# Kernel tuning notes

Measured on AMD Instinct MI355X. Metric: run time of the kernel, lower is better.

Reference implementation:

```python
import jax, jax.numpy as jnp
import numpy as np

EPS = 1e-5

def bn(x, gamma, beta, axes):
    # training-mode batchnorm over `axes`, channel axis = 1 (matches nn.BatchNorm1d/2d)
    mean = jnp.mean(x, axis=axes, keepdims=True)
    var = jnp.var(x, axis=axes, keepdims=True)
    shp = [1] * x.ndim
    shp[1] = -1
    return gamma.reshape(shp) * (x - mean) * jax.lax.rsqrt(var + EPS) + beta.reshape(shp)

def setup_inputs():
    key = jax.random.key(0)
    B, N, K, Cin, Cout, m = 4, 4096, 32, 64, 64, 8
    ks = jax.random.split(key, 10)
    def w(k, shape, fan_in):
        return jax.random.normal(k, shape, jnp.float32) * np.float32(np.sqrt(2.0 / fan_in))
    return {
        "x": jax.random.normal(ks[0], (B, Cin, N), jnp.float32),
        "xyz_score": jax.random.normal(ks[1], (B, 66, N, K), jnp.float32),
        "conv1_w": w(ks[2], (Cin, Cin), Cin),
        "bn1_g": jnp.ones((Cin,), jnp.float32), "bn1_b": jnp.zeros((Cin,), jnp.float32),
        "matrice2": w(ks[3], (Cin, m * Cout), Cin),  # weight bank: i x (m*o)
        "sn_w0": w(ks[4], (64, 66), 66), "sn_g0": jnp.ones((64,), jnp.float32), "sn_b0": jnp.zeros((64,), jnp.float32),
        "sn_w1": w(ks[5], (32, 64), 64), "sn_g1": jnp.ones((32,), jnp.float32), "sn_b1": jnp.zeros((32,), jnp.float32),
        "sn_w2": w(ks[6], (16, 32), 32), "sn_g2": jnp.ones((16,), jnp.float32), "sn_b2": jnp.zeros((16,), jnp.float32),
        "sn_w3": w(ks[7], (m, 16), 16), "sn_bias3": jnp.zeros((m,), jnp.float32),
        "bn2_g": jnp.ones((Cout,), jnp.float32), "bn2_b": jnp.zeros((Cout,), jnp.float32),
        "idx": jax.random.randint(ks[8], (B, N, K), 0, N, dtype=jnp.int32),
    }

def reference(x, xyz_score, conv1_w, bn1_g, bn1_b, matrice2,
              sn_w0, sn_g0, sn_b0, sn_w1, sn_g1, sn_b1, sn_w2, sn_g2, sn_b2,
              sn_w3, sn_bias3, bn2_g, bn2_b, idx):
    B, Cin, N = x.shape
    m = sn_w3.shape[0]
    # conv1 (1x1, no bias) + BN1 + ReLU  -> [B, Cin, N]
    h = jnp.einsum('oc,bcn->bon', conv1_w, x)
    h = jax.nn.relu(bn(h, bn1_g, bn1_b, (0, 2)))
    # feat_trans_pointnet: [B,N,Cin] @ [Cin, m*Cout] -> [B,N,m,Cout]
    y = jnp.einsum('bcn,ck->bnk', h, matrice2).reshape(B, N, m, -1)
    # ScoreNet: stack of 1x1 conv2d + BN + ReLU, final conv with bias, softmax over m
    s = xyz_score  # [B, 66, N, K]
    s = jax.nn.relu(bn(jnp.einsum('oc,bcnk->bonk', sn_w0, s), sn_g0, sn_b0, (0, 2, 3)))
    s = jax.nn.relu(bn(jnp.einsum('oc,bcnk->bonk', sn_w1, s), sn_g1, sn_b1, (0, 2, 3)))
    s = jax.nn.relu(bn(jnp.einsum('oc,bcnk->bonk', sn_w2, s), sn_g2, sn_b2, (0, 2, 3)))
    s = jnp.einsum('oc,bcnk->bonk', sn_w3, s) + sn_bias3[None, :, None, None]
    score = jax.nn.softmax(s, axis=1)            # [B, m, N, K], bias=0
    score = jnp.transpose(score, (0, 2, 3, 1))   # [B, N, K, m]
    # assemble_pointnet: gather neighbor transformed feats and score-weight them
    neigh = y[jnp.arange(B)[:, None, None], idx]             # [B, N, K, m, Cout]
    out = jnp.einsum('bnkm,bnkmo->bon', score, neigh)        # [B, Cout, N]
    return jax.nn.relu(bn(out, bn2_g, bn2_b, (0, 2)))
```

## Files before the change

### kernel.cpp

```cpp
#include <hip/hip_runtime.h>
#include <cstdint>

typedef unsigned short u16;
typedef unsigned int   u32;
typedef __attribute__((ext_vector_type(8))) short short8;
typedef __attribute__((ext_vector_type(4))) float f32x4;

constexpr int CB = 4;
constexpr int CN = 4096;
constexpr int CK = 32;
constexpr int NPTS = CB * CN * CK;
constexpr int NBK  = 131072;
constexpr float EPSV = 1e-5f;

struct __align__(16) Q4 { u32 a, b, c, d; };

static __device__ __forceinline__ u16 f2b(float f) {
  union { float f; u32 u; } v; v.f = f;
  u32 u = v.u;
  return (u16)((u + 0x7FFFu + ((u >> 16) & 1u)) >> 16);
}
static __device__ __forceinline__ float b2f(u16 h) {
  union { u32 u; float f; } v; v.u = ((u32)h) << 16;
  return v.f;
}
static __device__ __forceinline__ u32 pk2(float lo, float hi) {
  return (u32)f2b(lo) | ((u32)f2b(hi) << 16);
}
static __device__ __forceinline__ short8 mk8(u32 a, u32 b, u32 c, u32 d) {
  union { u32 w[4]; short8 v; } u; u.w[0]=a; u.w[1]=b; u.w[2]=c; u.w[3]=d; return u.v;
}

__global__ __launch_bounds__(256) void k_conv1(const float* __restrict__ x,
                                               const float* __restrict__ w,
                                               float* __restrict__ h,
                                               float* S, float* Q) {
  __shared__ float wl[16 * 64];
  __shared__ float ls[32];
  int tid = threadIdx.x;
  int og = blockIdx.x >> 6;
  int cb = blockIdx.x & 63;
  for (int i = tid; i < 1024; i += 256) wl[i] = w[og * 1024 + i];
  if (tid < 32) ls[tid] = 0.f;
  __syncthreads();
  int col = cb * 256 + tid;
  int b = col >> 12, n = col & 4095;
  float xr[64];
  const float* xp = x + (size_t)(b * 64) * CN + n;
  #pragma unroll
  for (int c = 0; c < 64; ++c) xr[c] = xp[(size_t)c * CN];
  int lane = tid & 63;
  for (int oo = 0; oo < 16; ++oo) {
    int o = og * 16 + oo;
    float acc = 0.f;
    const float* wr = &wl[oo * 64];
    #pragma unroll
    for (int c = 0; c < 64; ++c) acc = fmaf(wr[c], xr[c], acc);
    h[(size_t)(b * 64 + o) * CN + n] = acc;
    float v = acc, v2 = acc * acc;
    for (int d = 1; d < 64; d <<= 1) { v += __shfl_xor(v, d); v2 += __shfl_xor(v2, d); }
    if (lane == 0) { atomicAdd(&ls[oo], v); atomicAdd(&ls[16 + oo], v2); }
  }
  __syncthreads();
  if (tid < 16) atomicAdd(&S[og * 16 + tid], ls[tid]);
  else if (tid < 32) atomicAdd(&Q[og * 16 + tid - 16], ls[tid]);
}

__global__ __launch_bounds__(64) void k_affine(const float* S, const float* Q,
                                               const float* g, const float* bt,
                                               float* A, float* Bo, int C, float inv_cnt) {
  int t = threadIdx.x;
  if (t < C) {
    float mean = S[t] * inv_cnt;
    float var = fmaxf(Q[t] * inv_cnt - mean * mean, 0.f);
    float a = g[t] * rsqrtf(var + EPSV);
    A[t] = a;
    Bo[t] = bt[t] - mean * a;
  }
}

__global__ __launch_bounds__(256) void k_prepM2(const float* __restrict__ M2,
                                                u16* __restrict__ m2frag) {
  int i = blockIdx.x * 256 + threadIdx.x;
  int e = i & 7, lane = (i >> 3) & 63, t = i >> 9;
  int mt = t >> 1, kc = t & 1;
  int row = 16 * mt + (lane & 15);
  int k = 32 * kc + 8 * (lane >> 4) + e;
  m2frag[i] = f2b(M2[k * 512 + row]);
}

__global__ __launch_bounds__(256) void k_y(const float* __restrict__ h,
                                           const u16* __restrict__ m2frag,
                                           const float* __restrict__ Ah,
                                           const float* __restrict__ Bh,
                                           u16* __restrict__ y16) {
  __shared__ u16 yl[4][16 * 520];
  __shared__ float abl[128];
  int tid = threadIdx.x;
  if (tid < 64) abl[tid] = Ah[tid];
  else if (tid < 128) abl[tid] = Bh[tid - 64];
  int wv = tid >> 6, lane = tid & 63, g = lane >> 4, pl = lane & 15;
  __syncthreads();
  int wid = blockIdx.x * 4 + wv;
  int n0 = wid * 16;
  int b = n0 >> 12, nloc = n0 & 4095;
  const float* sb = h + (size_t)(b * 64) * CN + nloc + pl;
  u32 w[8];
  #pragma unroll
  for (int kc = 0; kc < 2; ++kc) {
    #pragma unroll
    for (int e2 = 0; e2 < 4; ++e2) {
      int c0 = 32 * kc + 8 * g + 2 * e2;
      float v0 = fmaxf(fmaf(abl[c0],     sb[(size_t)c0 * CN],       abl[64 + c0]),     0.f);
      float v1 = fmaxf(fmaf(abl[c0 + 1], sb[(size_t)(c0 + 1) * CN], abl[64 + c0 + 1]), 0.f);
      w[kc * 4 + e2] = pk2(v0, v1);
    }
  }
  short8 Bf0 = mk8(w[0], w[1], w[2], w[3]);
  short8 Bf1 = mk8(w[4], w[5], w[6], w[7]);
  const short8* m2f = (const short8*)m2frag;
  u16* ylw = &yl[wv][0];
  #pragma unroll
  for (int mt = 0; mt < 32; ++mt) {
    short8 A0 = m2f[(mt * 2 + 0) * 64 + lane];
    short8 A1 = m2f[(mt * 2 + 1) * 64 + lane];
    f32x4 z = {0.f, 0.f, 0.f, 0.f};
    z = __builtin_amdgcn_mfma_f32_16x16x32_bf16(A0, Bf0, z, 0, 0, 0);
    z = __builtin_amdgcn_mfma_f32_16x16x32_bf16(A1, Bf1, z, 0, 0, 0);
    u32* wp = (u32*)&ylw[pl * 520 + 16 * mt + 4 * g];
    wp[0] = pk2(z[0], z[1]);
    wp[1] = pk2(z[2], z[3]);
  }
  u16* yg = y16 + (size_t)n0 * 512;
  for (int j = 0; j < 16; ++j) {
    short8 v = *(const short8*)&ylw[j * 520 + lane * 8];
    *(short8*)(yg + (size_t)j * 512 + lane * 8) = v;
  }
}

static __device__ __forceinline__ void ld_frags(const float* __restrict__ xyz,
                                                int c, int g, int pl, short8 fr[5]) {
  int pbase = c * 32;
  int b = pbase >> 17, r = pbase & (NBK - 1);
  const float* base = xyz + (size_t)b * 66 * NBK + r + g * 8;
  #pragma unroll
  for (int ci = 0; ci < 4; ++ci) {
    const float* p = base + (size_t)(16 * ci + pl) * NBK;
    float4 v0 = *(const float4*)p;
    float4 v1 = *(const float4*)(p + 4);
    fr[ci] = mk8(pk2(v0.x, v0.y), pk2(v0.z, v0.w), pk2(v1.x, v1.y), pk2(v1.z, v1.w));
  }
  if (pl < 2) {
    const float* p = base + (size_t)(64 + pl) * NBK;
    float4 v0 = *(const float4*)p;
    float4 v1 = *(const float4*)(p + 4);
    fr[4] = mk8(pk2(v0.x, v0.y), pk2(v0.z, v0.w), pk2(v1.x, v1.y), pk2(v1.z, v1.w));
  } else if (pl == 2) {
    fr[4] = mk8(0x3F803F80u, 0x3F803F80u, 0x3F803F80u, 0x3F803F80u);
  } else {
    fr[4] = mk8(0u, 0u, 0u, 0u);
  }
}

__global__ __launch_bounds__(256) void k_moment(const float* __restrict__ xyz,
                                                float* __restrict__ Mpart) {
  constexpr int TI[15] = {0,0,0,0,0,1,1,1,1,2,2,2,3,3,4};
  constexpr int TJ[15] = {0,1,2,3,4,1,2,3,4,2,3,4,3,4,4};
  int tid = threadIdx.x;
  int wv = tid >> 6;
  int wid = blockIdx.x * 4 + wv;
  int lane = tid & 63, g = lane >> 4, pl = lane & 15;
  f32x4 acc[15];
  #pragma unroll
  for (int t = 0; t < 15; ++t) acc[t] = (f32x4){0.f, 0.f, 0.f, 0.f};
  for (int cc = wid; cc < NPTS / 32; cc += 4096) {
    short8 fr0[5], fr1[5];
    ld_frags(xyz, cc,        g, pl, fr0);
    ld_frags(xyz, cc + 2048, g, pl, fr1);
    #pragma unroll
    for (int t = 0; t < 15; ++t)
      acc[t] = __builtin_amdgcn_mfma_f32_16x16x32_bf16(fr0[TI[t]], fr0[TJ[t]], acc[t], 0, 0, 0);
    #pragma unroll
    for (int t = 0; t < 15; ++t)
      acc[t] = __builtin_amdgcn_mfma_f32_16x16x32_bf16(fr1[TI[t]], fr1[TJ[t]], acc[t], 0, 0, 0);
  }
  float* mp = Mpart + (size_t)wid * 3840;
  #pragma unroll
  for (int t = 0; t < 15; ++t)
    *(f32x4*)(mp + t * 256 + lane * 4) = acc[t];
}

__global__ __launch_bounds__(256) void k_mreduce(const float* __restrict__ Mpart,
                                                 float* __restrict__ M) {
  int e = blockIdx.x * 256 + threadIdx.x;
  int kg = blockIdx.y;
  float s = 0.f;
  for (int k = kg * 256; k < kg * 256 + 256; ++k) s += Mpart[(size_t)k * 3840 + e];
  atomicAdd(&M[e], s);
}

__global__ __launch_bounds__(256) void k_affine1m(const float* __restrict__ M,
                                                  const float* __restrict__ w0,
                                                  const float* __restrict__ g0,
                                                  const float* __restrict__ b0,
                                                  float* __restrict__ A1,
                                                  float* __restrict__ B1) {
  __shared__ float lsM[67 * 68];
  __shared__ float w0l[64 * 69];
  __shared__ float red[4 * 64];
  int tid = threadIdx.x;
  const float inv = 1.f / (float)NPTS;
  for (int i = tid; i < 67 * 67; i += 256) {
    int r = i / 67, c = i % 67;
    int rr = r, cc = c;
    if ((r >> 4) > (c >> 4)) { rr = c; cc = r; }
    int ti = rr >> 4, tj = cc >> 4;
    int t = ti * (9 - ti) / 2 + tj;
    int rho = rr & 15, kap = cc & 15;
    lsM[r * 68 + c] = M[t * 256 + ((rho >> 2) * 16 + kap) * 4 + (rho & 3)] * inv;
  }
  for (int i = tid; i < 64 * 66; i += 256) {
    int o = i / 66, c = i % 66;
    w0l[o * 69 + c] = w0[i];
  }
  __syncthreads();
  int o = tid & 63, sl = tid >> 6;
  float acc2 = 0.f;
  for (int c1 = sl * 17; c1 < sl * 17 + 17; ++c1) {
    if (c1 >= 66) break;
    float inner = 0.f;
    const float* mr = &lsM[c1 * 68];
    const float* wr = &w0l[o * 69];
    for (int c2 = 0; c2 < 66; ++c2) inner = fmaf(mr[c2], wr[c2], inner);
    acc2 = fmaf(wr[c1], inner, acc2);
  }
  red[sl * 64 + o] = acc2;
  __syncthreads();
  if (sl == 0) {
    float Ez2 = red[o] + red[64 + o] + red[128 + o] + red[192 + o];
    float mean = 0.f;
    const float* wr = &w0l[o * 69];
    for (int c = 0; c < 66; ++c) mean = fmaf(wr[c], lsM[c * 68 + 66], mean);
    float var = fmaxf(Ez2 - mean * mean, 0.f);
    float a = g0[o] * rsqrtf(var + EPSV);
    A1[o] = a;
    B1[o] = b0[o] - mean * a;
  }
}

__global__ __launch_bounds__(256) void k_prep(const float* __restrict__ w0,
                                              const float* __restrict__ w1,
                                              const float* __restrict__ A1,
                                              const float* __restrict__ B1,
                                              u16* __restrict__ w0frag,
                                              u16* __restrict__ w1frag) {
  int tid = threadIdx.x;
  for (int i = tid; i < 6144; i += 256) {
    int e = i & 7, lane = (i >> 3) & 63, t = i >> 9;
    int mt = t / 3, kc = t % 3;
    int row = 16 * mt + (lane & 15);
    int k = 32 * kc + 8 * (lane >> 4) + e;
    float v;
    if (k < 66)      v = A1[row] * w0[row * 66 + k];
    else if (k == 66) v = B1[row];
    else              v = 0.f;
    w0frag[i] = f2b(v);
  }
  for (int i = tid; i < 2048; i += 256) {
    int e = i & 7, lane = (i >> 3) & 63, t = i >> 9;
    int m2t = t >> 1, kc2 = t & 1;
    int row = 16 * m2t + (lane & 15);
    int k = 32 * kc2 + 8 * (lane >> 4) + e;
    w1frag[i] = f2b(w1[row * 64 + k]);
  }
}

__global__ __launch_bounds__(256) void k_s2(const float* __restrict__ xyz,
                                            const u16* __restrict__ w0frag,
                                            const u16* __restrict__ w1frag,
                                            u32* __restrict__ z2p,
                                            float* S, float* Q) {
  __shared__ u16 a1l[4][16][80];
  __shared__ float ls2[64];
  int tid = threadIdx.x;
  int wv = tid >> 6, lane = tid & 63, g = lane >> 4, pl = lane & 15;
  if (tid < 64) ls2[tid] = 0.f;
  __syncthreads();

  const short8* w0f = (const short8*)w0frag;
  const short8* w1f = (const short8*)w1frag;
  short8 A0[4][3];
  #pragma unroll
  for (int mt = 0; mt < 4; ++mt)
    #pragma unroll
    for (int kc = 0; kc < 3; ++kc) A0[mt][kc] = w0f[(mt * 3 + kc) * 64 + lane];
  short8 W1f[2][2];
  #pragma unroll
  for (int m2t = 0; m2t < 2; ++m2t)
    #pragma unroll
    for (int kc2 = 0; kc2 < 2; ++kc2) W1f[m2t][kc2] = w1f[(m2t * 2 + kc2) * 64 + lane];

  float sum8[8], sq8[8];
  #pragma unroll
  for (int i = 0; i < 8; ++i) { sum8[i] = 0.f; sq8[i] = 0.f; }

  int wid = blockIdx.x * 4 + wv;
  for (int s = wid; s < NPTS / 16; s += 8192) {
    int pg = s * 16;
    int b = pg >> 17, r = pg & (NBK - 1);
    const float* sb = xyz + (size_t)b * 66 * NBK + r + pl;
    float v[16];
    #pragma unroll
    for (int e = 0; e < 8; ++e) v[e]     = sb[(size_t)(8 * g + e) * NBK];
    #pragma unroll
    for (int e = 0; e < 8; ++e) v[8 + e] = sb[(size_t)(32 + 8 * g + e) * NBK];
    u32 c2a = 0u, c2b = 0u;
    if (g == 0) {
      float v64 = sb[(size_t)64 * NBK];
      float v65 = sb[(size_t)65 * NBK];
      c2a = pk2(v64, v65);
      c2b = 0x00003F80u;
    }
    short8 Bf0 = mk8(pk2(v[0], v[1]), pk2(v[2], v[3]), pk2(v[4], v[5]), pk2(v[6], v[7]));
    short8 Bf1 = mk8(pk2(v[8], v[9]), pk2(v[10], v[11]), pk2(v[12], v[13]), pk2(v[14], v[15]));
    short8 Bf2 = mk8(c2a, c2b, 0u, 0u);

    #pragma unroll
    for (int mt = 0; mt < 4; ++mt) {
      f32x4 z = {0.f, 0.f, 0.f, 0.f};
      z = __builtin_amdgcn_mfma_f32_16x16x32_bf16(A0[mt][0], Bf0, z, 0, 0, 0);
      z = __builtin_amdgcn_mfma_f32_16x16x32_bf16(A0[mt][1], Bf1, z, 0, 0, 0);
      z = __builtin_amdgcn_mfma_f32_16x16x32_bf16(A0[mt][2], Bf2, z, 0, 0, 0);
      float r0 = fmaxf(z[0], 0.f), r1 = fmaxf(z[1], 0.f);
      float r2 = fmaxf(z[2], 0.f), r3 = fmaxf(z[3], 0.f);
      u32* wp = (u32*)&a1l[wv][pl][16 * mt + 4 * g];
      wp[0] = pk2(r0, r1);
      wp[1] = pk2(r2, r3);
    }
    short8 B2f0 = *(const short8*)&a1l[wv][pl][8 * g];
    short8 B2f1 = *(const short8*)&a1l[wv][pl][32 + 8 * g];
    #pragma unroll
    for (int m2t = 0; m2t < 2; ++m2t) {
      f32x4 z2 = {0.f, 0.f, 0.f, 0.f};
      z2 = __builtin_amdgcn_mfma_f32_16x16x32_bf16(W1f[m2t][0], B2f0, z2, 0, 0, 0);
      z2 = __builtin_amdgcn_mfma_f32_16x16x32_bf16(W1f[m2t][1], B2f1, z2, 0, 0, 0);
      #pragma unroll
      for (int rr = 0; rr < 4; ++rr) {
        sum8[m2t * 4 + rr] += z2[rr];
        sq8[m2t * 4 + rr] += z2[rr] * z2[rr];
      }
      int jlo = 8 * m2t + 2 * g;
      z2p[(size_t)jlo * NPTS + pg + pl]       = pk2(z2[0], z2[1]);
      z2p[(size_t)(jlo + 1) * NPTS + pg + pl] = pk2(z2[2], z2[3]);
    }
  }
  #pragma unroll
  for (int i = 0; i < 8; ++i) {
    float vS = sum8[i], vQ = sq8[i];
    for (int d = 1; d < 16; d <<= 1) { vS += __shfl_xor(vS, d); vQ += __shfl_xor(vQ, d); }
    if (pl == 0) {
      int ch = 16 * (i >> 2) + 4 * g + (i & 3);
      atomicAdd(&ls2[ch], vS);
      atomicAdd(&ls2[32 + ch], vQ);
    }
  }
  __syncthreads();
  if (tid < 32) atomicAdd(&S[tid], ls2[tid]);
  else if (tid < 64) atomicAdd(&Q[tid - 32], ls2[tid]);
}

__global__ __launch_bounds__(256) void k_s3(const u32* __restrict__ z2p,
                                            const float* __restrict__ w2,
                                            const float* __restrict__ A2,
                                            const float* __restrict__ B2,
                                            u32* __restrict__ z3,
                                            float* S, float* Q) {
  __shared__ float w2l[16 * 32];
  __shared__ float ab[64];
  __shared__ float ls[32];
  int tid = threadIdx.x;
  for (int i = tid; i < 512; i += 256) w2l[i] = w2[i];
  if (tid < 32) { ab[tid] = A2[tid]; ls[tid] = 0.f; }
  else if (tid < 64) ab[tid] = B2[tid - 32];
  __syncthreads();
  int p = blockIdx.x * 256 + tid;
  float a2[32];
  #pragma unroll
  for (int j = 0; j < 16; ++j) {
    u32 wj = z2p[(size_t)j * NPTS + p];
    float lo = b2f((u16)(wj & 0xFFFFu));
    float hi = b2f((u16)(wj >> 16));
    a2[2 * j]     = fmaxf(fmaf(ab[2 * j], lo, ab[32 + 2 * j]), 0.f);
    a2[2 * j + 1] = fmaxf(fmaf(ab[2 * j + 1], hi, ab[32 + 2 * j + 1]), 0.f);
  }
  int lane = tid & 63;
  float zt[16];
  for (int j = 0; j < 16; ++j) {
    float z = 0.f;
    const float* wr = &w2l[j * 32];
    #pragma unroll
    for (int c = 0; c < 32; ++c) z = fmaf(wr[c], a2[c], z);
    zt[j] = z;
    float v = z, v2 = z * z;
    for (int d = 1; d < 64; d <<= 1) { v += __shfl_xor(v, d); v2 += __shfl_xor(v2, d); }
    if (lane == 0) { atomicAdd(&ls[j], v); atomicAdd(&ls[16 + j], v2); }
  }
  u32 pkk[8];
  #pragma unroll
  for (int j = 0; j < 8; ++j) pkk[j] = pk2(zt[2 * j], zt[2 * j + 1]);
  Q4* dst = (Q4*)(z3 + (size_t)p * 8);
  #pragma unroll
  for (int i = 0; i < 2; ++i) { Q4 q; q.a = pkk[4*i]; q.b = pkk[4*i+1]; q.c = pkk[4*i+2]; q.d = pkk[4*i+3]; dst[i] = q; }
  __syncthreads();
  if (tid < 16) atomicAdd(&S[tid], ls[tid]);
  else if (tid < 32) atomicAdd(&Q[tid - 16], ls[tid]);
}

__global__ __launch_bounds__(256) void k_score(const u32* __restrict__ z3,
                                               const float* __restrict__ w3,
                                               const float* __restrict__ bias3,
                                               const float* __restrict__ A3,
                                               const float* __restrict__ B3,
                                               float* __restrict__ scores) {
  __shared__ float w3l[128];
  __shared__ float bl[8];
  __shared__ float ab[32];
  int tid = threadIdx.x;
  if (tid < 128) w3l[tid] = w3[tid];
  if (tid < 8) bl[tid] = bias3[tid];
  if (tid < 16) ab[tid] = A3[tid];
  else if (tid < 32) ab[tid] = B3[tid - 16];
  __syncthreads();
  int p = blockIdx.x * 256 + tid;
  const Q4* zp = (const Q4*)(z3 + (size_t)p * 8);
  Q4 r0 = zp[0], r1 = zp[1];
  u32 w8[8] = {r0.a, r0.b, r0.c, r0.d, r1.a, r1.b, r1.c, r1.d};
  float a3[16];
  #pragma unroll
  for (int t = 0; t < 8; ++t) {
    int c = t * 2;
    a3[c]     = fmaxf(fmaf(ab[c], b2f((u16)(w8[t] & 0xFFFFu)), ab[16 + c]), 0.f);
    a3[c + 1] = fmaxf(fmaf(ab[c + 1], b2f((u16)(w8[t] >> 16)), ab[16 + c + 1]), 0.f);
  }
  float z4[8]; float mx = -1e30f;
  #pragma unroll
  for (int mI = 0; mI < 8; ++mI) {
    float z = bl[mI];
    const float* wr = &w3l[mI * 16];
    #pragma unroll
    for (int c = 0; c < 16; ++c) z = fmaf(wr[c], a3[c], z);
    z4[mI] = z; mx = fmaxf(mx, z);
  }
  float ssum = 0.f;
  #pragma unroll
  for (int mI = 0; mI < 8; ++mI) { z4[mI] = __expf(z4[mI] - mx); ssum += z4[mI]; }
  float inv = 1.f / ssum;
  float4* sp = (float4*)(scores + (size_t)p * 8);
  sp[0] = make_float4(z4[0] * inv, z4[1] * inv, z4[2] * inv, z4[3] * inv);
  sp[1] = make_float4(z4[4] * inv, z4[5] * inv, z4[6] * inv, z4[7] * inv);
}

__global__ __launch_bounds__(256) void k_gather(const u16* __restrict__ y16,
                                                const float* __restrict__ scores,
                                                const int* __restrict__ idx,
                                                float* __restrict__ out0,
                                                float* S, float* Q) {
  __shared__ float ls[128];
  int tid = threadIdx.x;
  if (tid < 128) ls[tid] = 0.f;
  __syncthreads();
  int bid = blockIdx.x;
  int batch = (bid & 7) >> 1;
  int sub = ((bid >> 3) << 1) | (bid & 1);
  int wv = tid >> 6, lane = tid & 63;
  int m = lane >> 3, og = lane & 7;
  const u16* ybase = y16 + (size_t)batch * CN * 512;
  int pid0 = (batch << 12) + sub * 8 + wv * 2;
  int pbase = pid0 * 32;
  int jv = idx[pbase + lane];
  float acc0[8] = {0, 0, 0, 0, 0, 0, 0, 0};
  float acc1[8] = {0, 0, 0, 0, 0, 0, 0, 0};
  #pragma unroll 4
  for (int k = 0; k < 32; ++k) {
    int j0 = __shfl(jv, k);
    int j1 = __shfl(jv, 32 + k);
    float s0 = scores[(size_t)(pbase + k) * 8 + m];
    float s1 = scores[(size_t)(pbase + 32 + k) * 8 + m];
    short8 y0 = *(const short8*)(ybase + ((size_t)j0 << 9) + lane * 8);
    short8 y1 = *(const short8*)(ybase + ((size_t)j1 << 9) + lane * 8);
    #pragma unroll
    for (int t = 0; t < 8; ++t) {
      acc0[t] = fmaf(s0, b2f((u16)y0[t]), acc0[t]);
      acc1[t] = fmaf(s1, b2f((u16)y1[t]), acc1[t]);
    }
  }
  #pragma unroll
  for (int d = 8; d < 64; d <<= 1) {
    #pragma unroll
    for (int t = 0; t < 8; ++t) {
      acc0[t] += __shfl_xor(acc0[t], d);
      acc1[t] += __shfl_xor(acc1[t], d);
    }
  }
  if (m == 0) {
    float* op0 = out0 + (size_t)pid0 * 64 + og * 8;
    *(float4*)op0       = make_float4(acc0[0], acc0[1], acc0[2], acc0[3]);
    *(float4*)(op0 + 4) = make_float4(acc0[4], acc0[5], acc0[6], acc0[7]);
    float* op1 = out0 + (size_t)(pid0 + 1) * 64 + og * 8;
    *(float4*)op1       = make_float4(acc1[0], acc1[1], acc1[2], acc1[3]);
    *(float4*)(op1 + 4) = make_float4(acc1[4], acc1[5], acc1[6], acc1[7]);
    #pragma unroll
    for (int t = 0; t < 8; ++t) {
      float sv = acc0[t] + acc1[t];
      float qv = acc0[t] * acc0[t] + acc1[t] * acc1[t];
      atomicAdd(&ls[og * 8 + t], sv);
      atomicAdd(&ls[64 + og * 8 + t], qv);
    }
  }
  __syncthreads();
  if (tid < 64) atomicAdd(&S[tid], ls[tid]);
  else if (tid < 128) atomicAdd(&Q[tid - 64], ls[tid]);
}

__global__ __launch_bounds__(256) void k_bn2(const float* __restrict__ out0,
                                             const float* __restrict__ A,
                                             const float* __restrict__ Bo,
                                             float* __restrict__ outp) {
  int gid = blockIdx.x * 256 + threadIdx.x;
  for (int i = gid; i < CB * 64 * CN; i += 262144) {
    int b = i >> 18, o = (i >> 12) & 63, n = i & 4095;
    float v = out0[((size_t)((b << 12) | n)) * 64 + o];
    outp[i] = fmaxf(fmaf(A[o], v, Bo[o]), 0.f);
  }
}

extern "C" void kernel_launch(void* const* d_in, const int* in_sizes, int n_in,
                              void* d_out, int out_size, void* d_ws, size_t ws_size,
                              hipStream_t stream) {
  const float* x       = (const float*)d_in[0];
  const float* xyz     = (const float*)d_in[1];
  const float* conv1_w = (const float*)d_in[2];
  const float* bn1_g   = (const float*)d_in[3];
  const float* bn1_b   = (const float*)d_in[4];
  const float* M2      = (const float*)d_in[5];
  const float* w0      = (const float*)d_in[6];
  const float* g0      = (const float*)d_in[7];
  const float* b0      = (const float*)d_in[8];
  const float* w1      = (const float*)d_in[9];
  const float* g1      = (const float*)d_in[10];
  const float* b1      = (const float*)d_in[11];
  const float* w2      = (const float*)d_in[12];
  const float* g2      = (const float*)d_in[13];
  const float* b2      = (const float*)d_in[14];
  const float* w3      = (const float*)d_in[15];
  const float* bias3   = (const float*)d_in[16];
  const float* bn2_g   = (const float*)d_in[17];
  const float* bn2_b   = (const float*)d_in[18];
  const int*   idx     = (const int*)d_in[19];
  float* out = (float*)d_out;

  char* wsb = (char*)d_ws;
  float* h      = (float*)wsb;
  u16*   y16    = (u16*)(wsb + 4194304);
  float* scores = (float*)(wsb + 20971520);
  u32*   z2p    = (u32*)(wsb + 37748736);
  u32*   z3     = (u32*)(wsb + 71303168);
  float* out0   = (float*)(wsb + 88080384);
  float* sums   = (float*)(wsb + 92274688);
  float* S_h = sums;        float* Q_h = sums + 64;
  float* S_2 = sums + 128;  float* Q_2 = sums + 160;
  float* S_3 = sums + 192;  float* Q_3 = sums + 208;
  float* S_o = sums + 224;  float* Q_o = sums + 288;
  float* Mm  = sums + 352;
  float* A_h = sums + 6752; float* B_h = sums + 6816;
  float* A_1 = sums + 6880; float* B_1 = sums + 6944;
  float* A_2 = sums + 7008; float* B_2 = sums + 7040;
  float* A_3 = sums + 7072; float* B_3 = sums + 7088;
  float* A_o = sums + 7104; float* B_o = sums + 7168;
  u16* w0frag = (u16*)(sums + 7232);
  u16* w1frag = w0frag + 6144;
  u16* m2frag = w1frag + 2048;
  float* Mpart = (float*)z2p;

  hipMemsetAsync(sums, 0, 6752 * sizeof(float), stream);

  k_prepM2<<<128, 256, 0, stream>>>(M2, m2frag);
  k_conv1<<<256, 256, 0, stream>>>(x, conv1_w, h, S_h, Q_h);
  k_affine<<<1, 64, 0, stream>>>(S_h, Q_h, bn1_g, bn1_b, A_h, B_h, 64, 1.f / 16384.f);
  k_y<<<256, 256, 0, stream>>>(h, m2frag, A_h, B_h, y16);

  k_moment<<<512, 256, 0, stream>>>(xyz, Mpart);
  k_mreduce<<<dim3(15, 8), 256, 0, stream>>>(Mpart, Mm);
  k_affine1m<<<1, 256, 0, stream>>>(Mm, w0, g0, b0, A_1, B_1);
  k_prep<<<1, 256, 0, stream>>>(w0, w1, A_1, B_1, w0frag, w1frag);
  k_s2<<<2048, 256, 0, stream>>>(xyz, w0frag, w1frag, z2p, S_2, Q_2);
  k_affine<<<1, 64, 0, stream>>>(S_2, Q_2, g1, b1, A_2, B_2, 32, 1.f / (float)NPTS);
  k_s3<<<2048, 256, 0, stream>>>(z2p, w2, A_2, B_2, z3, S_3, Q_3);
  k_affine<<<1, 64, 0, stream>>>(S_3, Q_3, g2, b2, A_3, B_3, 16, 1.f / (float)NPTS);

  k_score<<<2048, 256, 0, stream>>>(z3, w3, bias3, A_3, B_3, scores);
  k_gather<<<2048, 256, 0, stream>>>(y16, scores, idx, out0, S_o, Q_o);
  k_affine<<<1, 64, 0, stream>>>(S_o, Q_o, bn2_g, bn2_b, A_o, B_o, 64, 1.f / 16384.f);
  k_bn2<<<1024, 256, 0, stream>>>(out0, A_o, B_o, out);
}
```

Measured before the change: 312.1 us.

## Replace moment-matrix BN1 statistics with explicit two-pass layer-0 activation storage

Removes the xyz second-moment MFMA pass, its reduction and the analytic BN1 affine computation. Instead a new kernel computes raw layer-0 conv outputs, accumulates per-channel sum and sum of squares, and stores them in bf16 to a new workspace buffer. A second kernel reloads them, applies the BN1 affine plus ReLU, and proceeds with layer 1. This trades the extra full xyz read and moment math for writing and reading a 64-channel bf16 intermediate.

```diff
diff --git a/kernel.cpp b/kernel.cpp
--- a/kernel.cpp
+++ b/kernel.cpp
@@ -138,120 +138,8 @@
   }
 }
 
-static __device__ __forceinline__ void ld_frags(const float* __restrict__ xyz,
-                                                int c, int g, int pl, short8 fr[5]) {
-  int pbase = c * 32;
-  int b = pbase >> 17, r = pbase & (NBK - 1);
-  const float* base = xyz + (size_t)b * 66 * NBK + r + g * 8;
-  #pragma unroll
-  for (int ci = 0; ci < 4; ++ci) {
-    const float* p = base + (size_t)(16 * ci + pl) * NBK;
-    float4 v0 = *(const float4*)p;
-    float4 v1 = *(const float4*)(p + 4);
-    fr[ci] = mk8(pk2(v0.x, v0.y), pk2(v0.z, v0.w), pk2(v1.x, v1.y), pk2(v1.z, v1.w));
-  }
-  if (pl < 2) {
-    const float* p = base + (size_t)(64 + pl) * NBK;
-    float4 v0 = *(const float4*)p;
-    float4 v1 = *(const float4*)(p + 4);
-    fr[4] = mk8(pk2(v0.x, v0.y), pk2(v0.z, v0.w), pk2(v1.x, v1.y), pk2(v1.z, v1.w));
-  } else if (pl == 2) {
-    fr[4] = mk8(0x3F803F80u, 0x3F803F80u, 0x3F803F80u, 0x3F803F80u);
-  } else {
-    fr[4] = mk8(0u, 0u, 0u, 0u);
-  }
-}
-
-__global__ __launch_bounds__(256) void k_moment(const float* __restrict__ xyz,
-                                                float* __restrict__ Mpart) {
-  constexpr int TI[15] = {0,0,0,0,0,1,1,1,1,2,2,2,3,3,4};
-  constexpr int TJ[15] = {0,1,2,3,4,1,2,3,4,2,3,4,3,4,4};
-  int tid = threadIdx.x;
-  int wv = tid >> 6;
-  int wid = blockIdx.x * 4 + wv;
-  int lane = tid & 63, g = lane >> 4, pl = lane & 15;
-  f32x4 acc[15];
-  #pragma unroll
-  for (int t = 0; t < 15; ++t) acc[t] = (f32x4){0.f, 0.f, 0.f, 0.f};
-  for (int cc = wid; cc < NPTS / 32; cc += 4096) {
-    short8 fr0[5], fr1[5];
-    ld_frags(xyz, cc,        g, pl, fr0);
-    ld_frags(xyz, cc + 2048, g, pl, fr1);
-    #pragma unroll
-    for (int t = 0; t < 15; ++t)
-      acc[t] = __builtin_amdgcn_mfma_f32_16x16x32_bf16(fr0[TI[t]], fr0[TJ[t]], acc[t], 0, 0, 0);
-    #pragma unroll
-    for (int t = 0; t < 15; ++t)
-      acc[t] = __builtin_amdgcn_mfma_f32_16x16x32_bf16(fr1[TI[t]], fr1[TJ[t]], acc[t], 0, 0, 0);
-  }
-  float* mp = Mpart + (size_t)wid * 3840;
-  #pragma unroll
-  for (int t = 0; t < 15; ++t)
-    *(f32x4*)(mp + t * 256 + lane * 4) = acc[t];
-}
-
-__global__ __launch_bounds__(256) void k_mreduce(const float* __restrict__ Mpart,
-                                                 float* __restrict__ M) {
-  int e = blockIdx.x * 256 + threadIdx.x;
-  int kg = blockIdx.y;
-  float s = 0.f;
-  for (int k = kg * 256; k < kg * 256 + 256; ++k) s += Mpart[(size_t)k * 3840 + e];
-  atomicAdd(&M[e], s);
-}
-
-__global__ __launch_bounds__(256) void k_affine1m(const float* __restrict__ M,
-                                                  const float* __restrict__ w0,
-                                                  const float* __restrict__ g0,
-                                                  const float* __restrict__ b0,
-                                                  float* __restrict__ A1,
-                                                  float* __restrict__ B1) {
-  __shared__ float lsM[67 * 68];
-  __shared__ float w0l[64 * 69];
-  __shared__ float red[4 * 64];
-  int tid = threadIdx.x;
-  const float inv = 1.f / (float)NPTS;
-  for (int i = tid; i < 67 * 67; i += 256) {
-    int r = i / 67, c = i % 67;
-    int rr = r, cc = c;
-    if ((r >> 4) > (c >> 4)) { rr = c; cc = r; }
-    int ti = rr >> 4, tj = cc >> 4;
-    int t = ti * (9 - ti) / 2 + tj;
-    int rho = rr & 15, kap = cc & 15;
-    lsM[r * 68 + c] = M[t * 256 + ((rho >> 2) * 16 + kap) * 4 + (rho & 3)] * inv;
-  }
-  for (int i = tid; i < 64 * 66; i += 256) {
-    int o = i / 66, c = i % 66;
-    w0l[o * 69 + c] = w0[i];
-  }
-  __syncthreads();
-  int o = tid & 63, sl = tid >> 6;
-  float acc2 = 0.f;
-  for (int c1 = sl * 17; c1 < sl * 17 + 17; ++c1) {
-    if (c1 >= 66) break;
-    float inner = 0.f;
-    const float* mr = &lsM[c1 * 68];
-    const float* wr = &w0l[o * 69];
-    for (int c2 = 0; c2 < 66; ++c2) inner = fmaf(mr[c2], wr[c2], inner);
-    acc2 = fmaf(wr[c1], inner, acc2);
-  }
-  red[sl * 64 + o] = acc2;
-  __syncthreads();
-  if (sl == 0) {
-    float Ez2 = red[o] + red[64 + o] + red[128 + o] + red[192 + o];
-    float mean = 0.f;
-    const float* wr = &w0l[o * 69];
-    for (int c = 0; c < 66; ++c) mean = fmaf(wr[c], lsM[c * 68 + 66], mean);
-    float var = fmaxf(Ez2 - mean * mean, 0.f);
-    float a = g0[o] * rsqrtf(var + EPSV);
-    A1[o] = a;
-    B1[o] = b0[o] - mean * a;
-  }
-}
-
 __global__ __launch_bounds__(256) void k_prep(const float* __restrict__ w0,
                                               const float* __restrict__ w1,
-                                              const float* __restrict__ A1,
-                                              const float* __restrict__ B1,
                                               u16* __restrict__ w0frag,
                                               u16* __restrict__ w1frag) {
   int tid = threadIdx.x;
@@ -260,11 +148,7 @@
     int mt = t / 3, kc = t % 3;
     int row = 16 * mt + (lane & 15);
     int k = 32 * kc + 8 * (lane >> 4) + e;
-    float v;
-    if (k < 66)      v = A1[row] * w0[row * 66 + k];
-    else if (k == 66) v = B1[row];
-    else              v = 0.f;
-    w0frag[i] = f2b(v);
+    w0frag[i] = f2b(k < 66 ? w0[row * 66 + k] : 0.f);
   }
   for (int i = tid; i < 2048; i += 256) {
     int e = i & 7, lane = (i >> 3) & 63, t = i >> 9;
@@ -275,35 +159,25 @@
   }
 }
 
-__global__ __launch_bounds__(256) void k_s2(const float* __restrict__ xyz,
+__global__ __launch_bounds__(256) void k_s1(const float* __restrict__ xyz,
                                             const u16* __restrict__ w0frag,
-                                            const u16* __restrict__ w1frag,
-                                            u32* __restrict__ z2p,
+                                            u16* __restrict__ z1g,
                                             float* S, float* Q) {
   __shared__ u16 a1l[4][16][80];
-  __shared__ float ls2[64];
+  __shared__ float ls1[128];
   int tid = threadIdx.x;
   int wv = tid >> 6, lane = tid & 63, g = lane >> 4, pl = lane & 15;
-  if (tid < 64) ls2[tid] = 0.f;
-  __syncthreads();
-
+  if (tid < 128) ls1[tid] = 0.f;
+  __syncthreads();
   const short8* w0f = (const short8*)w0frag;
-  const short8* w1f = (const short8*)w1frag;
   short8 A0[4][3];
   #pragma unroll
   for (int mt = 0; mt < 4; ++mt)
     #pragma unroll
     for (int kc = 0; kc < 3; ++kc) A0[mt][kc] = w0f[(mt * 3 + kc) * 64 + lane];
-  short8 W1f[2][2];
-  #pragma unroll
-  for (int m2t = 0; m2t < 2; ++m2t)
-    #pragma unroll
-    for (int kc2 = 0; kc2 < 2; ++kc2) W1f[m2t][kc2] = w1f[(m2t * 2 + kc2) * 64 + lane];
-
-  float sum8[8], sq8[8];
-  #pragma unroll
-  for (int i = 0; i < 8; ++i) { sum8[i] = 0.f; sq8[i] = 0.f; }
-
+  float sum16[16], sq16[16];
+  #pragma unroll
+  for (int i = 0; i < 16; ++i) { sum16[i] = 0.f; sq16[i] = 0.f; }
   int wid = blockIdx.x * 4 + wv;
   for (int s = wid; s < NPTS / 16; s += 8192) {
     int pg = s * 16;
@@ -314,31 +188,94 @@
     for (int e = 0; e < 8; ++e) v[e]     = sb[(size_t)(8 * g + e) * NBK];
     #pragma unroll
     for (int e = 0; e < 8; ++e) v[8 + e] = sb[(size_t)(32 + 8 * g + e) * NBK];
-    u32 c2a = 0u, c2b = 0u;
+    u32 c2a = 0u;
     if (g == 0) {
       float v64 = sb[(size_t)64 * NBK];
       float v65 = sb[(size_t)65 * NBK];
       c2a = pk2(v64, v65);
-      c2b = 0x00003F80u;
     }
     short8 Bf0 = mk8(pk2(v[0], v[1]), pk2(v[2], v[3]), pk2(v[4], v[5]), pk2(v[6], v[7]));
     short8 Bf1 = mk8(pk2(v[8], v[9]), pk2(v[10], v[11]), pk2(v[12], v[13]), pk2(v[14], v[15]));
-    short8 Bf2 = mk8(c2a, c2b, 0u, 0u);
-
+    short8 Bf2 = mk8(c2a, 0u, 0u, 0u);
     #pragma unroll
     for (int mt = 0; mt < 4; ++mt) {
       f32x4 z = {0.f, 0.f, 0.f, 0.f};
       z = __builtin_amdgcn_mfma_f32_16x16x32_bf16(A0[mt][0], Bf0, z, 0, 0, 0);
       z = __builtin_amdgcn_mfma_f32_16x16x32_bf16(A0[mt][1], Bf1, z, 0, 0, 0);
       z = __builtin_amdgcn_mfma_f32_16x16x32_bf16(A0[mt][2], Bf2, z, 0, 0, 0);
-      float r0 = fmaxf(z[0], 0.f), r1 = fmaxf(z[1], 0.f);
-      float r2 = fmaxf(z[2], 0.f), r3 = fmaxf(z[3], 0.f);
+      #pragma unroll
+      for (int rr = 0; rr < 4; ++rr) {
+        sum16[mt * 4 + rr] += z[rr];
+        sq16[mt * 4 + rr] += z[rr] * z[rr];
+      }
       u32* wp = (u32*)&a1l[wv][pl][16 * mt + 4 * g];
-      wp[0] = pk2(r0, r1);
-      wp[1] = pk2(r2, r3);
-    }
-    short8 B2f0 = *(const short8*)&a1l[wv][pl][8 * g];
-    short8 B2f1 = *(const short8*)&a1l[wv][pl][32 + 8 * g];
+      wp[0] = pk2(z[0], z[1]);
+      wp[1] = pk2(z[2], z[3]);
+    }
+    int pt = lane >> 2, q = lane & 3;
+    short8 s0 = *(const short8*)&a1l[wv][pt][q * 16];
+    short8 s1 = *(const short8*)&a1l[wv][pt][q * 16 + 8];
+    u16* zg = z1g + ((size_t)(pg + pt)) * 64 + q * 16;
+    *(short8*)zg       = s0;
+    *(short8*)(zg + 8) = s1;
+  }
+  #pragma unroll
+  for (int i = 0; i < 16; ++i) {
+    float vS = sum16[i], vQ = sq16[i];
+    for (int d = 1; d < 16; d <<= 1) { vS += __shfl_xor(vS, d); vQ += __shfl_xor(vQ, d); }
+    if (pl == 0) {
+      int ch = 16 * (i >> 2) + 4 * g + (i & 3);
+      atomicAdd(&ls1[ch], vS);
+      atomicAdd(&ls1[64 + ch], vQ);
+    }
+  }
+  __syncthreads();
+  if (tid < 64) atomicAdd(&S[tid], ls1[tid]);
+  else if (tid < 128) atomicAdd(&Q[tid - 64], ls1[tid]);
+}
+
+__global__ __launch_bounds__(256) void k_s2b(const u16* __restrict__ z1g,
+                                             const u16* __restrict__ w1frag,
+                                             const float* __restrict__ A1,
+                                             const float* __restrict__ B1,
+                                             u32* __restrict__ z2p,
+                                             float* S, float* Q) {
+  __shared__ float ab[128];
+  __shared__ float ls2[64];
+  int tid = threadIdx.x;
+  int wv = tid >> 6, lane = tid & 63, g = lane >> 4, pl = lane & 15;
+  if (tid < 64) { ab[tid] = A1[tid]; ls2[tid] = 0.f; }
+  else if (tid < 128) ab[tid] = B1[tid - 64];
+  __syncthreads();
+  const short8* w1f = (const short8*)w1frag;
+  short8 W1f[2][2];
+  #pragma unroll
+  for (int m2t = 0; m2t < 2; ++m2t)
+    #pragma unroll
+    for (int kc2 = 0; kc2 < 2; ++kc2) W1f[m2t][kc2] = w1f[(m2t * 2 + kc2) * 64 + lane];
+  float sum8[8], sq8[8];
+  #pragma unroll
+  for (int i = 0; i < 8; ++i) { sum8[i] = 0.f; sq8[i] = 0.f; }
+  int wid = blockIdx.x * 4 + wv;
+  for (int s = wid; s < NPTS / 16; s += 8192) {
+    int pg = s * 16;
+    const u16* zr = z1g + ((size_t)(pg + pl)) * 64 + 8 * g;
+    short8 r0 = *(const short8*)zr;
+    short8 r1 = *(const short8*)(zr + 32);
+    u32 wa[4], wb[4];
+    #pragma unroll
+    for (int e2 = 0; e2 < 4; ++e2) {
+      int c0 = 8 * g + 2 * e2;
+      float v0 = fmaxf(fmaf(ab[c0],     b2f((u16)r0[2 * e2]),     ab[64 + c0]),     0.f);
+      float v1 = fmaxf(fmaf(ab[c0 + 1], b2f((u16)r0[2 * e2 + 1]), ab[64 + c0 + 1]), 0.f);
+      wa[e2] = pk2(v0, v1);
+      int c1 = 32 + 8 * g + 2 * e2;
+      float v2 = fmaxf(fmaf(ab[c1],     b2f((u16)r1[2 * e2]),     ab[64 + c1]),     0.f);
+      float v3 = fmaxf(fmaf(ab[c1 + 1], b2f((u16)r1[2 * e2 + 1]), ab[64 + c1 + 1]), 0.f);
+      wb[e2] = pk2(v2, v3);
+    }
+    short8 B2f0 = mk8(wa[0], wa[1], wa[2], wa[3]);
+    short8 B2f1 = mk8(wb[0], wb[1], wb[2], wb[3]);
     #pragma unroll
     for (int m2t = 0; m2t < 2; ++m2t) {
       f32x4 z2 = {0.f, 0.f, 0.f, 0.f};
@@ -567,33 +504,33 @@
   u32*   z3     = (u32*)(wsb + 71303168);
   float* out0   = (float*)(wsb + 88080384);
   float* sums   = (float*)(wsb + 92274688);
+  u16*   z1g    = (u16*)(wsb + 100663296);
   float* S_h = sums;        float* Q_h = sums + 64;
-  float* S_2 = sums + 128;  float* Q_2 = sums + 160;
-  float* S_3 = sums + 192;  float* Q_3 = sums + 208;
-  float* S_o = sums + 224;  float* Q_o = sums + 288;
-  float* Mm  = sums + 352;
-  float* A_h = sums + 6752; float* B_h = sums + 6816;
-  float* A_1 = sums + 6880; float* B_1 = sums + 6944;
-  float* A_2 = sums + 7008; float* B_2 = sums + 7040;
-  float* A_3 = sums + 7072; float* B_3 = sums + 7088;
-  float* A_o = sums + 7104; float* B_o = sums + 7168;
-  u16* w0frag = (u16*)(sums + 7232);
+  float* S_1 = sums + 128;  float* Q_1 = sums + 192;
+  float* S_2 = sums + 256;  float* Q_2 = sums + 288;
+  float* S_3 = sums + 320;  float* Q_3 = sums + 336;
+  float* S_o = sums + 352;  float* Q_o = sums + 416;
+  float* aff = sums + 480;
+  float* A_h = aff;        float* B_h = aff + 64;
+  float* A_1 = aff + 128;  float* B_1 = aff + 192;
+  float* A_2 = aff + 256;  float* B_2 = aff + 288;
+  float* A_3 = aff + 320;  float* B_3 = aff + 336;
+  float* A_o = aff + 352;  float* B_o = aff + 416;
+  u16* w0frag = (u16*)(sums + 960);
   u16* w1frag = w0frag + 6144;
   u16* m2frag = w1frag + 2048;
-  float* Mpart = (float*)z2p;
-
-  hipMemsetAsync(sums, 0, 6752 * sizeof(float), stream);
+
+  hipMemsetAsync(sums, 0, 480 * sizeof(float), stream);
 
   k_prepM2<<<128, 256, 0, stream>>>(M2, m2frag);
+  k_prep<<<1, 256, 0, stream>>>(w0, w1, w0frag, w1frag);
   k_conv1<<<256, 256, 0, stream>>>(x, conv1_w, h, S_h, Q_h);
   k_affine<<<1, 64, 0, stream>>>(S_h, Q_h, bn1_g, bn1_b, A_h, B_h, 64, 1.f / 16384.f);
   k_y<<<256, 256, 0, stream>>>(h, m2frag, A_h, B_h, y16);
 
-  k_moment<<<512, 256, 0, stream>>>(xyz, Mpart);
-  k_mreduce<<<dim3(15, 8), 256, 0, stream>>>(Mpart, Mm);
-  k_affine1m<<<1, 256, 0, stream>>>(Mm, w0, g0, b0, A_1, B_1);
-  k_prep<<<1, 256, 0, stream>>>(w0, w1, A_1, B_1, w0frag, w1frag);
-  k_s2<<<2048, 256, 0, stream>>>(xyz, w0frag, w1frag, z2p, S_2, Q_2);
+  k_s1<<<2048, 256, 0, stream>>>(xyz, w0frag, z1g, S_1, Q_1);
+  k_affine<<<1, 64, 0, stream>>>(S_1, Q_1, g0, b0, A_1, B_1, 64, 1.f / (float)NPTS);
+  k_s2b<<<2048, 256, 0, stream>>>(z1g, w1frag, A_1, B_1, z2p, S_2, Q_2);
   k_affine<<<1, 64, 0, stream>>>(S_2, Q_2, g1, b1, A_2, B_2, 32, 1.f / (float)NPTS);
   k_s3<<<2048, 256, 0, stream>>>(z2p, w2, A_2, B_2, z3, S_3, Q_3);
   k_affine<<<1, 64, 0, stream>>>(S_3, Q_3, g2, b2, A_3, B_3, 16, 1.f / (float)NPTS);
```

Result: slower. 331.2 us (+6.1%).
